# Performance work log

Hardware: AMD Instinct MI355X
Metric: run time of the kernel (lower is better)

Reference implementation:

```python
import jax, jax.numpy as jnp
from jax import lax
import numpy as np

INPUT_SIZE = 64
HIDDEN = 16
SEQ_LEN = 512
NUM_CLASSES = 6
BATCH = 1024


def setup_inputs() -> dict:
    key = jax.random.key(0)
    ks = jax.random.split(key, 7)
    s_ih = 1.0 / np.sqrt(HIDDEN)
    return {
        "x": jax.random.normal(ks[0], (BATCH, SEQ_LEN, INPUT_SIZE), dtype=jnp.float32),
        # PyTorch LSTM params: gate order [i, f, g, o]
        "w_ih": jax.random.uniform(ks[1], (4 * HIDDEN, INPUT_SIZE), minval=-s_ih, maxval=s_ih, dtype=jnp.float32),
        "w_hh": jax.random.uniform(ks[2], (4 * HIDDEN, HIDDEN), minval=-s_ih, maxval=s_ih, dtype=jnp.float32),
        "b_ih": jax.random.uniform(ks[3], (4 * HIDDEN,), minval=-s_ih, maxval=s_ih, dtype=jnp.float32),
        "b_hh": jax.random.uniform(ks[4], (4 * HIDDEN,), minval=-s_ih, maxval=s_ih, dtype=jnp.float32),
        "w_fc": jax.random.uniform(ks[5], (NUM_CLASSES, HIDDEN * SEQ_LEN),
                                   minval=-1.0 / np.sqrt(HIDDEN * SEQ_LEN),
                                   maxval=1.0 / np.sqrt(HIDDEN * SEQ_LEN), dtype=jnp.float32),
        "b_fc": jax.random.uniform(ks[6], (NUM_CLASSES,),
                                   minval=-1.0 / np.sqrt(HIDDEN * SEQ_LEN),
                                   maxval=1.0 / np.sqrt(HIDDEN * SEQ_LEN), dtype=jnp.float32),
    }


def reference(x, w_ih, w_hh, b_ih, b_hh, w_fc, b_fc):
    B, T, _ = x.shape
    H = w_hh.shape[1]
    # Precompute input contribution to all gates: [B, T, 4H]
    gates_x = jnp.einsum("bti,gi->btg", x, w_ih) + b_ih + b_hh
    gates_t = jnp.swapaxes(gates_x, 0, 1)  # [T, B, 4H] for scan

    def step(carry, gx):
        h, c = carry
        g = gx + h @ w_hh.T  # [B, 4H]
        i, f, gg, o = jnp.split(g, 4, axis=-1)
        c = jax.nn.sigmoid(f) * c + jax.nn.sigmoid(i) * jnp.tanh(gg)
        h = jax.nn.sigmoid(o) * jnp.tanh(c)
        return (h, c), h

    h0 = jnp.zeros((B, H), x.dtype)
    _, hs = lax.scan(step, (h0, h0), gates_t)  # hs: [T, B, H]
    out = jnp.swapaxes(hs, 0, 1).reshape(B, T * H)  # flatten per batch_first reshape
    return out @ w_fc.T + b_fc
```

## Files before the change

### kernel.cpp

```cpp
#include <hip/hip_runtime.h>
#include <stdint.h>

#define SEQ   512
#define NB    1024
#define NIN   64
#define NH    16
#define NCLS  6
#define GSTRIDE 20

typedef __attribute__((ext_vector_type(8))) short short8;
typedef __attribute__((ext_vector_type(4))) float f32x4;

__device__ __forceinline__ float readlane_f(float v, int l) {
    return __int_as_float(__builtin_amdgcn_readlane(__float_as_int(v), l));
}

__device__ __forceinline__ void split8(float4 u0, float4 u1, short8& hi, short8& lo) {
    float f[8] = {u0.x, u0.y, u0.z, u0.w, u1.x, u1.y, u1.z, u1.w};
    #pragma unroll
    for (int j = 0; j < 8; ++j) {
        uint32_t b = __float_as_uint(f[j]);
        uint16_t hb = (uint16_t)(b >> 16);
        hi[j] = (short)hb;
        float hf = __uint_as_float(((uint32_t)hb) << 16);
        lo[j] = (short)(uint16_t)(__float_as_uint(f[j] - hf) >> 16);
    }
}

__device__ __forceinline__ float quad_bcast0(float v) {
    return __int_as_float(__builtin_amdgcn_update_dpp(0, __float_as_int(v), 0x00, 0xF, 0xF, true));
}
__device__ __forceinline__ float quad_bcast1(float v) {
    return __int_as_float(__builtin_amdgcn_update_dpp(0, __float_as_int(v), 0x55, 0xF, 0xF, true));
}
__device__ __forceinline__ float quad_bcast2(float v) {
    return __int_as_float(__builtin_amdgcn_update_dpp(0, __float_as_int(v), 0xAA, 0xF, 0xF, true));
}
__device__ __forceinline__ float quad_bcast3(float v) {
    return __int_as_float(__builtin_amdgcn_update_dpp(0, __float_as_int(v), 0xFF, 0xF, 0xF, true));
}

__global__ __launch_bounds__(256, 1)
void lstm_fused_kernel(const float* __restrict__ x,
                       const float* __restrict__ w_ih,
                       const float* __restrict__ w_hh,
                       const float* __restrict__ b_ih,
                       const float* __restrict__ b_hh,
                       const float* __restrict__ w_fc,
                       const float* __restrict__ b_fc,
                       float* __restrict__ out)
{
    __shared__ float stageG[4][64 * GSTRIDE];
    __shared__ float stageHT[4][256];

    const int tid  = threadIdx.x;
    const int wid  = tid >> 6;
    const int lane = tid & 63;
    const int b    = blockIdx.x * 4 + wid;

    const int ml   = lane & 15;
    const int half = lane >> 4;
    const int kk   = half * 8;

    short8 Bh[4][2], Bl[4][2];
    #pragma unroll
    for (int tau = 0; tau < 4; ++tau) {
        #pragma unroll
        for (int ch = 0; ch < 2; ++ch) {
            const float* wr = w_ih + (tau * 16 + ml) * NIN + ch * 32 + kk;
            float4 u0 = *(const float4*)wr;
            float4 u1 = *(const float4*)(wr + 4);
            split8(u0, u1, Bh[tau][ch], Bl[tau][ch]);
        }
    }

    float bw[4];
    #pragma unroll
    for (int tau = 0; tau < 4; ++tau)
        bw[tau] = b_ih[tau * 16 + ml] + b_hh[tau * 16 + ml];

    const int gate_t = lane & 3;
    const int u      = lane >> 2;
    const int grow   = gate_t * 16 + u;
    float whh[NH];
    #pragma unroll
    for (int j = 0; j < NH; j += 4) {
        float4 w4 = *(const float4*)(w_hh + grow * NH + j);
        whh[j] = w4.x; whh[j+1] = w4.y; whh[j+2] = w4.z; whh[j+3] = w4.w;
    }

    const bool  isg = (gate_t == 2);
    const float sA  = isg ? 2.f : 1.f;
    const float sB  = isg ? -1.f : 0.f;
    const float nk  = sA * -1.4426950408889634f;

    float c_state = 0.f;
    float hs[NH];
    #pragma unroll
    for (int j = 0; j < NH; ++j) hs[j] = 0.f;
    float accfc[NCLS];
    #pragma unroll
    for (int cls = 0; cls < NCLS; ++cls) accfc[cls] = 0.f;

    const float* xbase = x + ((size_t)b * SEQ + ml) * NIN + kk;
    float4 px0 = *(const float4*)(xbase + 0);
    float4 px1 = *(const float4*)(xbase + 4);
    float4 px2 = *(const float4*)(xbase + 32);
    float4 px3 = *(const float4*)(xbase + 36);

    for (int grp = 0; grp < SEQ / 16; ++grp) {
        float4 wf[NCLS];
        #pragma unroll
        for (int cls = 0; cls < NCLS; ++cls)
            wf[cls] = *(const float4*)(w_fc + cls * (SEQ * NH) + grp * 256 + lane * 4);

        short8 a0h, a0l, a1h, a1l;
        split8(px0, px1, a0h, a0l);
        split8(px2, px3, a1h, a1l);

        if (grp < SEQ / 16 - 1) {
            const float* xp = xbase + (size_t)(grp + 1) * 16 * NIN;
            px0 = *(const float4*)(xp + 0);
            px1 = *(const float4*)(xp + 4);
            px2 = *(const float4*)(xp + 32);
            px3 = *(const float4*)(xp + 36);
        }

        f32x4 acc[4];
        #pragma unroll
        for (int tau = 0; tau < 4; ++tau) {
            f32x4 c_ = {0.f, 0.f, 0.f, 0.f};
            c_ = __builtin_amdgcn_mfma_f32_16x16x32_bf16(a0h, Bh[tau][0], c_, 0, 0, 0);
            c_ = __builtin_amdgcn_mfma_f32_16x16x32_bf16(a1h, Bh[tau][1], c_, 0, 0, 0);
            c_ = __builtin_amdgcn_mfma_f32_16x16x32_bf16(a0l, Bh[tau][0], c_, 0, 0, 0);
            c_ = __builtin_amdgcn_mfma_f32_16x16x32_bf16(a0h, Bl[tau][0], c_, 0, 0, 0);
            c_ = __builtin_amdgcn_mfma_f32_16x16x32_bf16(a1l, Bh[tau][1], c_, 0, 0, 0);
            c_ = __builtin_amdgcn_mfma_f32_16x16x32_bf16(a1h, Bl[tau][1], c_, 0, 0, 0);
            acc[tau] = c_;
        }

        #pragma unroll
        for (int tau = 0; tau < 4; ++tau) {
            f32x4 a4 = acc[tau];
            a4[0] += bw[tau]; a4[1] += bw[tau]; a4[2] += bw[tau]; a4[3] += bw[tau];
            *(f32x4*)&stageG[wid][(ml * 4 + tau) * GSTRIDE + half * 4] = a4;
        }
        __builtin_amdgcn_s_waitcnt(0xC07F);

        float gvv[16];
        #pragma unroll
        for (int q = 0; q < 4; ++q) {
            f32x4 g4 = *(f32x4*)&stageG[wid][lane * GSTRIDE + q * 4];
            gvv[q*4+0] = g4[0]; gvv[q*4+1] = g4[1]; gvv[q*4+2] = g4[2]; gvv[q*4+3] = g4[3];
        }

        #pragma unroll
        for (int r = 0; r < 16; ++r) {
            float q0 = fmaf(hs[0], whh[0], gvv[r]);
            float q1 = hs[1] * whh[1];
            float q2 = hs[2] * whh[2];
            float q3 = hs[3] * whh[3];
            #pragma unroll
            for (int j = 4; j < NH; j += 4) {
                q0 = fmaf(hs[j+0], whh[j+0], q0);
                q1 = fmaf(hs[j+1], whh[j+1], q1);
                q2 = fmaf(hs[j+2], whh[j+2], q2);
                q3 = fmaf(hs[j+3], whh[j+3], q3);
            }
            const float gatev = (q0 + q1) + (q2 + q3);

            const float e   = __builtin_amdgcn_exp2f(gatev * nk);
            const float act = fmaf(sA, __builtin_amdgcn_rcpf(1.f + e), sB);

            const float ig = quad_bcast0(act);
            const float fg = quad_bcast1(act);
            const float gg = quad_bcast2(act);
            const float og = quad_bcast3(act);

            c_state = fmaf(fg, c_state, ig * gg);
            const float e2 = __builtin_amdgcn_exp2f(c_state * -2.8853900817779268f);
            const float th = fmaf(2.f, __builtin_amdgcn_rcpf(1.f + e2), -1.f);
            const float hn = og * th;

            if ((lane & 3) == 0) stageHT[wid][r * NH + u] = hn;

            #pragma unroll
            for (int j = 0; j < NH; ++j) hs[j] = readlane_f(hn, 4 * j);
        }
        __builtin_amdgcn_s_waitcnt(0xC07F);

        {
            float4 h4 = *(float4*)&stageHT[wid][lane * 4];
            #pragma unroll
            for (int cls = 0; cls < NCLS; ++cls) {
                accfc[cls] = fmaf(h4.x, wf[cls].x, accfc[cls]);
                accfc[cls] = fmaf(h4.y, wf[cls].y, accfc[cls]);
                accfc[cls] = fmaf(h4.z, wf[cls].z, accfc[cls]);
                accfc[cls] = fmaf(h4.w, wf[cls].w, accfc[cls]);
            }
        }
    }

    #pragma unroll
    for (int cls = 0; cls < NCLS; ++cls) {
        float v = accfc[cls];
        v += __shfl_xor(v, 1);
        v += __shfl_xor(v, 2);
        v += __shfl_xor(v, 4);
        v += __shfl_xor(v, 8);
        v += __shfl_xor(v, 16);
        v += __shfl_xor(v, 32);
        accfc[cls] = v;
    }
    if (lane == 0) {
        #pragma unroll
        for (int cls = 0; cls < NCLS; ++cls)
            out[b * NCLS + cls] = accfc[cls] + b_fc[cls];
    }
}

extern "C" void kernel_launch(void* const* d_in, const int* in_sizes, int n_in,
                              void* d_out, int out_size, void* d_ws, size_t ws_size,
                              hipStream_t stream) {
    const float* x    = (const float*)d_in[0];
    const float* w_ih = (const float*)d_in[1];
    const float* w_hh = (const float*)d_in[2];
    const float* b_ih = (const float*)d_in[3];
    const float* b_hh = (const float*)d_in[4];
    const float* w_fc = (const float*)d_in[5];
    const float* b_fc = (const float*)d_in[6];
    float* out = (float*)d_out;

    hipLaunchKernelGGL(lstm_fused_kernel, dim3(NB / 4), dim3(256), 0, stream,
                       x, w_ih, w_hh, b_ih, b_hh, w_fc, b_fc, out);
}
```

Before: 239.2 us.

## Split LSTM into producer/consumer warp-specialized waves with double-buffered LDS

Each block now runs 8 waves: 4 producer waves compute the input-gate projections with MFMA and the FC accumulation, and 4 consumer waves run the serial recurrence. Gate tiles and hidden-state tiles are double-buffered in shared memory and handed over with block barriers once per 16-step group. The intent is to take the x-projection, global loads and FC work off the recurrence's critical path. The cost is a block-wide __syncthreads per group coupling all four sequences and doubled wave count per block.

Measured after the change: 238.8 us. About the same (-0.2%).

```diff
diff --git a/kernel.cpp b/kernel.cpp
--- a/kernel.cpp
+++ b/kernel.cpp
@@ -7,6 +7,7 @@
 #define NH    16
 #define NCLS  6
 #define GSTRIDE 20
+#define NGRP  (SEQ / 16)
 
 typedef __attribute__((ext_vector_type(8))) short short8;
 typedef __attribute__((ext_vector_type(4))) float f32x4;
@@ -40,182 +41,216 @@
     return __int_as_float(__builtin_amdgcn_update_dpp(0, __float_as_int(v), 0xFF, 0xF, 0xF, true));
 }
 
-__global__ __launch_bounds__(256, 1)
-void lstm_fused_kernel(const float* __restrict__ x,
-                       const float* __restrict__ w_ih,
-                       const float* __restrict__ w_hh,
-                       const float* __restrict__ b_ih,
-                       const float* __restrict__ b_hh,
-                       const float* __restrict__ w_fc,
-                       const float* __restrict__ b_fc,
-                       float* __restrict__ out)
+__global__ __launch_bounds__(512, 2)
+void lstm_ws_kernel(const float* __restrict__ x,
+                    const float* __restrict__ w_ih,
+                    const float* __restrict__ w_hh,
+                    const float* __restrict__ b_ih,
+                    const float* __restrict__ b_hh,
+                    const float* __restrict__ w_fc,
+                    const float* __restrict__ b_fc,
+                    float* __restrict__ out)
 {
-    __shared__ float stageG[4][64 * GSTRIDE];
-    __shared__ float stageHT[4][256];
+    __shared__ float G [4][2][64 * GSTRIDE];
+    __shared__ float HT[4][2][16 * NH];
 
     const int tid  = threadIdx.x;
     const int wid  = tid >> 6;
     const int lane = tid & 63;
-    const int b    = blockIdx.x * 4 + wid;
-
-    const int ml   = lane & 15;
-    const int half = lane >> 4;
-    const int kk   = half * 8;
-
-    short8 Bh[4][2], Bl[4][2];
-    #pragma unroll
-    for (int tau = 0; tau < 4; ++tau) {
-        #pragma unroll
-        for (int ch = 0; ch < 2; ++ch) {
-            const float* wr = w_ih + (tau * 16 + ml) * NIN + ch * 32 + kk;
-            float4 u0 = *(const float4*)wr;
-            float4 u1 = *(const float4*)(wr + 4);
-            split8(u0, u1, Bh[tau][ch], Bl[tau][ch]);
-        }
-    }
-
-    float bw[4];
-    #pragma unroll
-    for (int tau = 0; tau < 4; ++tau)
-        bw[tau] = b_ih[tau * 16 + ml] + b_hh[tau * 16 + ml];
-
-    const int gate_t = lane & 3;
-    const int u      = lane >> 2;
-    const int grow   = gate_t * 16 + u;
-    float whh[NH];
-    #pragma unroll
-    for (int j = 0; j < NH; j += 4) {
-        float4 w4 = *(const float4*)(w_hh + grow * NH + j);
-        whh[j] = w4.x; whh[j+1] = w4.y; whh[j+2] = w4.z; whh[j+3] = w4.w;
-    }
-
-    const bool  isg = (gate_t == 2);
-    const float sA  = isg ? 2.f : 1.f;
-    const float sB  = isg ? -1.f : 0.f;
-    const float nk  = sA * -1.4426950408889634f;
-
-    float c_state = 0.f;
-    float hs[NH];
-    #pragma unroll
-    for (int j = 0; j < NH; ++j) hs[j] = 0.f;
-    float accfc[NCLS];
-    #pragma unroll
-    for (int cls = 0; cls < NCLS; ++cls) accfc[cls] = 0.f;
-
-    const float* xbase = x + ((size_t)b * SEQ + ml) * NIN + kk;
-    float4 px0 = *(const float4*)(xbase + 0);
-    float4 px1 = *(const float4*)(xbase + 4);
-    float4 px2 = *(const float4*)(xbase + 32);
-    float4 px3 = *(const float4*)(xbase + 36);
-
-    for (int grp = 0; grp < SEQ / 16; ++grp) {
-        float4 wf[NCLS];
-        #pragma unroll
-        for (int cls = 0; cls < NCLS; ++cls)
-            wf[cls] = *(const float4*)(w_fc + cls * (SEQ * NH) + grp * 256 + lane * 4);
-
-        short8 a0h, a0l, a1h, a1l;
-        split8(px0, px1, a0h, a0l);
-        split8(px2, px3, a1h, a1l);
-
-        if (grp < SEQ / 16 - 1) {
-            const float* xp = xbase + (size_t)(grp + 1) * 16 * NIN;
+    const int e    = wid & 3;
+    const int b    = blockIdx.x * 4 + e;
+    const bool producer = (wid < 4);
+
+    if (producer) {
+        const int ml   = lane & 15;
+        const int half = lane >> 4;
+        const int kk   = half * 8;
+
+        short8 Bh[4][2], Bl[4][2];
+        #pragma unroll
+        for (int tau = 0; tau < 4; ++tau) {
+            #pragma unroll
+            for (int ch = 0; ch < 2; ++ch) {
+                const float* wr = w_ih + (tau * 16 + ml) * NIN + ch * 32 + kk;
+                float4 u0 = *(const float4*)wr;
+                float4 u1 = *(const float4*)(wr + 4);
+                split8(u0, u1, Bh[tau][ch], Bl[tau][ch]);
+            }
+        }
+        float bw[4];
+        #pragma unroll
+        for (int tau = 0; tau < 4; ++tau)
+            bw[tau] = b_ih[tau * 16 + ml] + b_hh[tau * 16 + ml];
+
+        const float* xbase = x + ((size_t)b * SEQ + ml) * NIN + kk;
+        float4 px0 = *(const float4*)(xbase + 0);
+        float4 px1 = *(const float4*)(xbase + 4);
+        float4 px2 = *(const float4*)(xbase + 32);
+        float4 px3 = *(const float4*)(xbase + 36);
+
+        {
+            short8 a0h, a0l, a1h, a1l;
+            split8(px0, px1, a0h, a0l);
+            split8(px2, px3, a1h, a1l);
+            #pragma unroll
+            for (int tau = 0; tau < 4; ++tau) {
+                f32x4 c_ = {0.f, 0.f, 0.f, 0.f};
+                c_ = __builtin_amdgcn_mfma_f32_16x16x32_bf16(a0h, Bh[tau][0], c_, 0, 0, 0);
+                c_ = __builtin_amdgcn_mfma_f32_16x16x32_bf16(a1h, Bh[tau][1], c_, 0, 0, 0);
+                c_ = __builtin_amdgcn_mfma_f32_16x16x32_bf16(a0l, Bh[tau][0], c_, 0, 0, 0);
+                c_ = __builtin_amdgcn_mfma_f32_16x16x32_bf16(a0h, Bl[tau][0], c_, 0, 0, 0);
+                c_ = __builtin_amdgcn_mfma_f32_16x16x32_bf16(a1l, Bh[tau][1], c_, 0, 0, 0);
+                c_ = __builtin_amdgcn_mfma_f32_16x16x32_bf16(a1h, Bl[tau][1], c_, 0, 0, 0);
+                c_[0] += bw[tau]; c_[1] += bw[tau]; c_[2] += bw[tau]; c_[3] += bw[tau];
+                *(f32x4*)&G[e][0][(ml * 4 + tau) * GSTRIDE + half * 4] = c_;
+            }
+        }
+        {
+            const float* xp = xbase + (size_t)16 * NIN;
             px0 = *(const float4*)(xp + 0);
             px1 = *(const float4*)(xp + 4);
             px2 = *(const float4*)(xp + 32);
             px3 = *(const float4*)(xp + 36);
         }
-
-        f32x4 acc[4];
-        #pragma unroll
-        for (int tau = 0; tau < 4; ++tau) {
-            f32x4 c_ = {0.f, 0.f, 0.f, 0.f};
-            c_ = __builtin_amdgcn_mfma_f32_16x16x32_bf16(a0h, Bh[tau][0], c_, 0, 0, 0);
-            c_ = __builtin_amdgcn_mfma_f32_16x16x32_bf16(a1h, Bh[tau][1], c_, 0, 0, 0);
-            c_ = __builtin_amdgcn_mfma_f32_16x16x32_bf16(a0l, Bh[tau][0], c_, 0, 0, 0);
-            c_ = __builtin_amdgcn_mfma_f32_16x16x32_bf16(a0h, Bl[tau][0], c_, 0, 0, 0);
-            c_ = __builtin_amdgcn_mfma_f32_16x16x32_bf16(a1l, Bh[tau][1], c_, 0, 0, 0);
-            c_ = __builtin_amdgcn_mfma_f32_16x16x32_bf16(a1h, Bl[tau][1], c_, 0, 0, 0);
-            acc[tau] = c_;
-        }
-
-        #pragma unroll
-        for (int tau = 0; tau < 4; ++tau) {
-            f32x4 a4 = acc[tau];
-            a4[0] += bw[tau]; a4[1] += bw[tau]; a4[2] += bw[tau]; a4[3] += bw[tau];
-            *(f32x4*)&stageG[wid][(ml * 4 + tau) * GSTRIDE + half * 4] = a4;
-        }
-        __builtin_amdgcn_s_waitcnt(0xC07F);
-
-        float gvv[16];
-        #pragma unroll
-        for (int q = 0; q < 4; ++q) {
-            f32x4 g4 = *(f32x4*)&stageG[wid][lane * GSTRIDE + q * 4];
-            gvv[q*4+0] = g4[0]; gvv[q*4+1] = g4[1]; gvv[q*4+2] = g4[2]; gvv[q*4+3] = g4[3];
-        }
-
-        #pragma unroll
-        for (int r = 0; r < 16; ++r) {
-            float q0 = fmaf(hs[0], whh[0], gvv[r]);
-            float q1 = hs[1] * whh[1];
-            float q2 = hs[2] * whh[2];
-            float q3 = hs[3] * whh[3];
-            #pragma unroll
-            for (int j = 4; j < NH; j += 4) {
-                q0 = fmaf(hs[j+0], whh[j+0], q0);
-                q1 = fmaf(hs[j+1], whh[j+1], q1);
-                q2 = fmaf(hs[j+2], whh[j+2], q2);
-                q3 = fmaf(hs[j+3], whh[j+3], q3);
-            }
-            const float gatev = (q0 + q1) + (q2 + q3);
-
-            const float e   = __builtin_amdgcn_exp2f(gatev * nk);
-            const float act = fmaf(sA, __builtin_amdgcn_rcpf(1.f + e), sB);
-
-            const float ig = quad_bcast0(act);
-            const float fg = quad_bcast1(act);
-            const float gg = quad_bcast2(act);
-            const float og = quad_bcast3(act);
-
-            c_state = fmaf(fg, c_state, ig * gg);
-            const float e2 = __builtin_amdgcn_exp2f(c_state * -2.8853900817779268f);
-            const float th = fmaf(2.f, __builtin_amdgcn_rcpf(1.f + e2), -1.f);
-            const float hn = og * th;
-
-            if ((lane & 3) == 0) stageHT[wid][r * NH + u] = hn;
-
-            #pragma unroll
-            for (int j = 0; j < NH; ++j) hs[j] = readlane_f(hn, 4 * j);
-        }
-        __builtin_amdgcn_s_waitcnt(0xC07F);
+        __syncthreads();
+
+        float accfc[NCLS];
+        #pragma unroll
+        for (int cls = 0; cls < NCLS; ++cls) accfc[cls] = 0.f;
+
+        for (int g = 0; g < NGRP; ++g) {
+            if (g < NGRP - 1) {
+                short8 a0h, a0l, a1h, a1l;
+                split8(px0, px1, a0h, a0l);
+                split8(px2, px3, a1h, a1l);
+                if (g < NGRP - 2) {
+                    const float* xp = xbase + (size_t)(g + 2) * 16 * NIN;
+                    px0 = *(const float4*)(xp + 0);
+                    px1 = *(const float4*)(xp + 4);
+                    px2 = *(const float4*)(xp + 32);
+                    px3 = *(const float4*)(xp + 36);
+                }
+                #pragma unroll
+                for (int tau = 0; tau < 4; ++tau) {
+                    f32x4 c_ = {0.f, 0.f, 0.f, 0.f};
+                    c_ = __builtin_amdgcn_mfma_f32_16x16x32_bf16(a0h, Bh[tau][0], c_, 0, 0, 0);
+                    c_ = __builtin_amdgcn_mfma_f32_16x16x32_bf16(a1h, Bh[tau][1], c_, 0, 0, 0);
+                    c_ = __builtin_amdgcn_mfma_f32_16x16x32_bf16(a0l, Bh[tau][0], c_, 0, 0, 0);
+                    c_ = __builtin_amdgcn_mfma_f32_16x16x32_bf16(a0h, Bl[tau][0], c_, 0, 0, 0);
+                    c_ = __builtin_amdgcn_mfma_f32_16x16x32_bf16(a1l, Bh[tau][1], c_, 0, 0, 0);
+                    c_ = __builtin_amdgcn_mfma_f32_16x16x32_bf16(a1h, Bl[tau][1], c_, 0, 0, 0);
+                    c_[0] += bw[tau]; c_[1] += bw[tau]; c_[2] += bw[tau]; c_[3] += bw[tau];
+                    *(f32x4*)&G[e][(g + 1) & 1][(ml * 4 + tau) * GSTRIDE + half * 4] = c_;
+                }
+            }
+            if (g > 0) {
+                const int gp = g - 1;
+                float4 h4 = *(float4*)&HT[e][gp & 1][lane * 4];
+                #pragma unroll
+                for (int cls = 0; cls < NCLS; ++cls) {
+                    float4 wf = *(const float4*)(w_fc + cls * (SEQ * NH) + gp * 256 + lane * 4);
+                    accfc[cls] = fmaf(h4.x, wf.x, accfc[cls]);
+                    accfc[cls] = fmaf(h4.y, wf.y, accfc[cls]);
+                    accfc[cls] = fmaf(h4.z, wf.z, accfc[cls]);
+                    accfc[cls] = fmaf(h4.w, wf.w, accfc[cls]);
+                }
+            }
+            __syncthreads();
+        }
 
         {
-            float4 h4 = *(float4*)&stageHT[wid][lane * 4];
+            const int gp = NGRP - 1;
+            float4 h4 = *(float4*)&HT[e][gp & 1][lane * 4];
             #pragma unroll
             for (int cls = 0; cls < NCLS; ++cls) {
-                accfc[cls] = fmaf(h4.x, wf[cls].x, accfc[cls]);
-                accfc[cls] = fmaf(h4.y, wf[cls].y, accfc[cls]);
-                accfc[cls] = fmaf(h4.z, wf[cls].z, accfc[cls]);
-                accfc[cls] = fmaf(h4.w, wf[cls].w, accfc[cls]);
-            }
-        }
-    }
-
-    #pragma unroll
-    for (int cls = 0; cls < NCLS; ++cls) {
-        float v = accfc[cls];
-        v += __shfl_xor(v, 1);
-        v += __shfl_xor(v, 2);
-        v += __shfl_xor(v, 4);
-        v += __shfl_xor(v, 8);
-        v += __shfl_xor(v, 16);
-        v += __shfl_xor(v, 32);
-        accfc[cls] = v;
-    }
-    if (lane == 0) {
-        #pragma unroll
-        for (int cls = 0; cls < NCLS; ++cls)
-            out[b * NCLS + cls] = accfc[cls] + b_fc[cls];
+                float4 wf = *(const float4*)(w_fc + cls * (SEQ * NH) + gp * 256 + lane * 4);
+                accfc[cls] = fmaf(h4.x, wf.x, accfc[cls]);
+                accfc[cls] = fmaf(h4.y, wf.y, accfc[cls]);
+                accfc[cls] = fmaf(h4.z, wf.z, accfc[cls]);
+                accfc[cls] = fmaf(h4.w, wf.w, accfc[cls]);
+            }
+        }
+        #pragma unroll
+        for (int cls = 0; cls < NCLS; ++cls) {
+            float v = accfc[cls];
+            v += __shfl_xor(v, 1);
+            v += __shfl_xor(v, 2);
+            v += __shfl_xor(v, 4);
+            v += __shfl_xor(v, 8);
+            v += __shfl_xor(v, 16);
+            v += __shfl_xor(v, 32);
+            accfc[cls] = v;
+        }
+        if (lane == 0) {
+            #pragma unroll
+            for (int cls = 0; cls < NCLS; ++cls)
+                out[b * NCLS + cls] = accfc[cls] + b_fc[cls];
+        }
+    } else {
+        const int gate_t = lane & 3;
+        const int u      = lane >> 2;
+        const int grow   = gate_t * 16 + u;
+        float whh[NH];
+        #pragma unroll
+        for (int j = 0; j < NH; j += 4) {
+            float4 w4 = *(const float4*)(w_hh + grow * NH + j);
+            whh[j] = w4.x; whh[j+1] = w4.y; whh[j+2] = w4.z; whh[j+3] = w4.w;
+        }
+        const bool  isg = (gate_t == 2);
+        const float sA  = isg ? 2.f : 1.f;
+        const float sB  = isg ? -1.f : 0.f;
+        const float nk  = sA * -1.4426950408889634f;
+
+        float c_state = 0.f;
+        float hs[NH];
+        #pragma unroll
+        for (int j = 0; j < NH; ++j) hs[j] = 0.f;
+
+        __syncthreads();
+
+        for (int g = 0; g < NGRP; ++g) {
+            float gvv[16];
+            #pragma unroll
+            for (int q = 0; q < 4; ++q) {
+                f32x4 g4 = *(f32x4*)&G[e][g & 1][lane * GSTRIDE + q * 4];
+                gvv[q*4+0] = g4[0]; gvv[q*4+1] = g4[1]; gvv[q*4+2] = g4[2]; gvv[q*4+3] = g4[3];
+            }
+
+            #pragma unroll
+            for (int r = 0; r < 16; ++r) {
+                float q0 = fmaf(hs[0], whh[0], gvv[r]);
+                float q1 = hs[1] * whh[1];
+                float q2 = hs[2] * whh[2];
+                float q3 = hs[3] * whh[3];
+                #pragma unroll
+                for (int j = 4; j < NH; j += 4) {
+                    q0 = fmaf(hs[j+0], whh[j+0], q0);
+                    q1 = fmaf(hs[j+1], whh[j+1], q1);
+                    q2 = fmaf(hs[j+2], whh[j+2], q2);
+                    q3 = fmaf(hs[j+3], whh[j+3], q3);
+                }
+                const float gatev = (q0 + q1) + (q2 + q3);
+
+                const float ex  = __builtin_amdgcn_exp2f(gatev * nk);
+                const float act = fmaf(sA, __builtin_amdgcn_rcpf(1.f + ex), sB);
+
+                const float ig = quad_bcast0(act);
+                const float fg = quad_bcast1(act);
+                const float gg = quad_bcast2(act);
+                const float og = quad_bcast3(act);
+
+                c_state = fmaf(fg, c_state, ig * gg);
+                const float e2 = __builtin_amdgcn_exp2f(c_state * -2.8853900817779268f);
+                const float th = fmaf(2.f, __builtin_amdgcn_rcpf(1.f + e2), -1.f);
+                const float hn = og * th;
+
+                HT[e][g & 1][r * NH + u] = hn;
+
+                #pragma unroll
+                for (int j = 0; j < NH; ++j) hs[j] = readlane_f(hn, 4 * j);
+            }
+            __syncthreads();
+        }
     }
 }
 
@@ -231,6 +266,6 @@
     const float* b_fc = (const float*)d_in[6];
     float* out = (float*)d_out;
 
-    hipLaunchKernelGGL(lstm_fused_kernel, dim3(NB / 4), dim3(256), 0, stream,
+    hipLaunchKernelGGL(lstm_ws_kernel, dim3(NB / 4), dim3(512), 0, stream,
                        x, w_ih, w_hh, b_ih, b_hh, w_fc, b_fc, out);
 }
```
